# Optimization experiments

Hardware: AMD Instinct MI355X
Metric: run time of the kernel (lower is better)

## Reference

```python
import jax, jax.numpy as jnp
import numpy as np

HIDDEN = 4096
N_HEADS = 32
N_KV = 8
HEAD_DIM = HIDDEN // N_HEADS  # 128
Q_SIZE = N_HEADS * HEAD_DIM   # 4096
KV_SIZE = N_KV * HEAD_DIM     # 1024
ROPE_THETA = 10000.0
B, S = 2, 2048


def _rope_cos_sin(positions):
    # positions: [B,S] int. inv_freq: [HEAD_DIM//2]
    inv_freq = 1.0 / (ROPE_THETA ** (jnp.arange(0, HEAD_DIM, 2, dtype=jnp.float32) / HEAD_DIM))
    ang = positions.astype(jnp.float32)[..., None] * inv_freq  # [B,S,D/2]
    return jnp.cos(ang), jnp.sin(ang)


def _apply_rope_neox(x, cos, sin):
    # x: [B,S,H,D]; neox style: rotate halves
    d2 = HEAD_DIM // 2
    x1, x2 = x[..., :d2], x[..., d2:]
    c = cos[:, :, None, :]
    s = sin[:, :, None, :]
    return jnp.concatenate([x1 * c - x2 * s, x2 * c + x1 * s], axis=-1)


def setup_inputs() -> dict:
    key = jax.random.key(0)
    k1, k2, k3 = jax.random.split(key, 3)
    positions = jnp.broadcast_to(jnp.arange(S, dtype=jnp.int32), (B, S))
    hidden_states = jax.random.normal(k1, (B, S, HIDDEN), dtype=jnp.float32)
    w_qkv = jax.random.normal(k2, (HIDDEN, Q_SIZE + 2 * KV_SIZE), dtype=jnp.float32) * (HIDDEN ** -0.5)
    w_o = jax.random.normal(k3, (Q_SIZE, HIDDEN), dtype=jnp.float32) * (Q_SIZE ** -0.5)
    return {"positions": positions, "hidden_states": hidden_states, "w_qkv": w_qkv, "w_o": w_o}


def reference(positions, hidden_states, w_qkv, w_o):
    qkv = hidden_states @ w_qkv  # [B,S,6144]
    q, k, v = jnp.split(qkv, [Q_SIZE, Q_SIZE + KV_SIZE], axis=-1)
    q = q.reshape(B, S, N_HEADS, HEAD_DIM)
    k = k.reshape(B, S, N_KV, HEAD_DIM)
    v = v.reshape(B, S, N_KV, HEAD_DIM)

    cos, sin = _rope_cos_sin(positions)
    q = _apply_rope_neox(q, cos, sin)
    k = _apply_rope_neox(k, cos, sin)

    # GQA: repeat kv heads to match query heads
    rep = N_HEADS // N_KV
    k = jnp.repeat(k, rep, axis=2)  # [B,S,H,D]
    v = jnp.repeat(v, rep, axis=2)

    scale = HEAD_DIM ** -0.5
    scores = jnp.einsum('bqhd,bkhd->bhqk', q, k) * scale  # [B,H,S,S]
    causal = jnp.tril(jnp.ones((S, S), dtype=bool))
    scores = jnp.where(causal[None, None], scores, jnp.float32(-1e30))
    probs = jax.nn.softmax(scores, axis=-1)
    attn = jnp.einsum('bhqk,bkhd->bqhd', probs, v).reshape(B, S, Q_SIZE)
    return attn @ w_o  # [B,S,HIDDEN]
```

## Files before the change

### kernel.cpp

```cpp
#include <hip/hip_runtime.h>
#include <stdint.h>
#include <stddef.h>


typedef short short8 __attribute__((ext_vector_type(8)));
typedef float f32x4  __attribute__((ext_vector_type(4)));

__device__ __forceinline__ float bf2f(short s) {
    union { uint32_t u; float f; } v;
    v.u = ((uint32_t)(uint16_t)s) << 16;
    return v.f;
}
__device__ __forceinline__ short f2bf(float f) {
    union { float f; uint32_t u; } v;
    v.f = f;
    uint32_t u = v.u;
    uint32_t r = (u + 0x7FFFu + ((u >> 16) & 1u)) >> 16;
    return (short)(uint16_t)r;
}
__device__ __forceinline__ short8 ldcvt8(const float* p) {
    float4 a = *(const float4*)p;
    float4 b = *(const float4*)(p + 4);
    short8 r;
    r[0] = f2bf(a.x); r[1] = f2bf(a.y); r[2] = f2bf(a.z); r[3] = f2bf(a.w);
    r[4] = f2bf(b.x); r[5] = f2bf(b.y); r[6] = f2bf(b.z); r[7] = f2bf(b.w);
    return r;
}
__device__ __forceinline__ void st_out(short* p, float v) { *p = f2bf(v); }
__device__ __forceinline__ void st_out(float* p, float v) { *p = v; }

#define GLDS16(g, l) __builtin_amdgcn_global_load_lds( \
    (const __attribute__((address_space(1))) void*)(g), \
    (__attribute__((address_space(3))) void*)(l), 16, 0, 0)

__global__ __launch_bounds__(256)
void cvt_bf16(const float* __restrict__ in, short* __restrict__ out, int n8)
{
    int i = blockIdx.x * 256 + threadIdx.x;
    int stride = gridDim.x * 256;
    for (; i < n8; i += stride)
        *(short8*)(out + (size_t)i * 8) = ldcvt8(in + (size_t)i * 8);
}

__global__ __launch_bounds__(256)
void transpose_cvt(const float* __restrict__ in, int ldin,
                   short* __restrict__ out, int R, int Cs)
{
    __shared__ short tile[64][72];
    const int bc = blockIdx.x * 64;
    const int br = blockIdx.y * 64;
    const int tid = threadIdx.x;
    const int r  = tid >> 2;
    const int c0 = (tid & 3) * 16;

    const float* src = in + (size_t)(br + r) * ldin + bc + c0;
#pragma unroll
    for (int i = 0; i < 4; i++) {
        float4 v = *(const float4*)(src + 4 * i);
        tile[c0 + 4 * i + 0][r] = f2bf(v.x);
        tile[c0 + 4 * i + 1][r] = f2bf(v.y);
        tile[c0 + 4 * i + 2][r] = f2bf(v.z);
        tile[c0 + 4 * i + 3][r] = f2bf(v.w);
    }
    __syncthreads();

    short* dst = out + (size_t)(bc + r) * R + br + c0;
    *(short8*)(dst)     = *(const short8*)(&tile[r][c0]);
    *(short8*)(dst + 8) = *(const short8*)(&tile[r][c0 + 8]);
}

__global__ __launch_bounds__(256)
void transpose_v(const short* __restrict__ qkv, short* __restrict__ vT)
{
    __shared__ short tile[64][72];
    const int bh = blockIdx.z;
    const int b  = bh >> 3;
    const int hk = bh & 7;
    const int s0 = blockIdx.x * 64;
    const int d0 = blockIdx.y * 64;
    const int tid = threadIdx.x;
    const int r  = tid >> 2;
    const int c0 = (tid & 3) * 16;

    const short* src = qkv + (size_t)(b * 2048 + s0 + r) * 6144 + 5120 + hk * 128 + d0 + c0;
    short8 v0 = *(const short8*)(src);
    short8 v1 = *(const short8*)(src + 8);
#pragma unroll
    for (int i = 0; i < 8; i++) tile[c0 + i][r] = v0[i];
#pragma unroll
    for (int i = 0; i < 8; i++) tile[c0 + 8 + i][r] = v1[i];
    __syncthreads();

    short* dst = vT + ((size_t)bh * 128 + d0 + r) * 2048 + s0 + c0;
    *(short8*)(dst)     = *(const short8*)(&tile[r][c0]);
    *(short8*)(dst + 8) = *(const short8*)(&tile[r][c0 + 8]);
}

__device__ __forceinline__ void stage_tile(const float* __restrict__ Ab, size_t lda,
                                           int kb, short* T, int tid)
{
    const int aRow = tid >> 3;
    const int aChk = tid & 7;
#pragma unroll
    for (int j = 0; j < 4; j++) {
        int row = aRow + 32 * j;
        short8 v = ldcvt8(Ab + (size_t)row * lda + kb + aChk * 8);
        *(short8*)(&T[row * 64 + ((aChk ^ (row & 7)) * 8)]) = v;
    }
}
__device__ __forceinline__ void stage_tile(const short* __restrict__ Ab, size_t lda,
                                           int kb, short* T, int tid)
{
    const int lane = tid & 63;
    const int wave = tid >> 6;
    const int sRow = lane >> 3;
    const int sPhy = lane & 7;
    const int logc = sPhy ^ sRow;
#pragma unroll
    for (int j = 0; j < 4; j++) {
        int row = wave * 32 + j * 8 + sRow;
        const short* g = Ab + (size_t)row * lda + kb + logc * 8;
        GLDS16(g, T + (size_t)(wave * 32 + j * 8) * 64);
    }
}

template <typename AT, typename CT>
__global__ __launch_bounds__(256, 2)
void gemm_tn(const AT* __restrict__ A, int lda, const short* __restrict__ Bt,
             CT* __restrict__ C, int ldc, int M, int N, int K)
{
    __shared__ __align__(16) short As[128 * 64];
    __shared__ __align__(16) short Bs[128 * 64];

    const int tid  = threadIdx.x;
    const int lane = tid & 63;
    const int wave = tid >> 6;
    const int l16  = lane & 15;
    const int quad = lane >> 4;
    const int wm   = wave >> 1;
    const int wn   = wave & 1;

    const int nbx = gridDim.x;
    const int nwg = nbx * gridDim.y;
    int wg = blockIdx.y * nbx + blockIdx.x;
    if ((nwg & 7) == 0) {
        const int cpx = nwg >> 3;
        wg = (wg & 7) * cpx + (wg >> 3);
    }
    const int mb = wg / nbx;
    const int nb = wg - mb * nbx;

    const AT*    Ab = A  + (size_t)mb * 128 * lda;
    const short* Bb = Bt + (size_t)nb * 128 * K;

    f32x4 acc[4][4];
#pragma unroll
    for (int i = 0; i < 4; i++)
#pragma unroll
        for (int j = 0; j < 4; j++) acc[i][j] = {0.f, 0.f, 0.f, 0.f};

    for (int kb = 0; kb < K; kb += 64) {
        __syncthreads();
        stage_tile(Ab, (size_t)lda, kb, As, tid);
        stage_tile(Bb, (size_t)K,   kb, Bs, tid);
        __syncthreads();

#pragma unroll
        for (int ks = 0; ks < 2; ks++) {
            short8 af[4], bf[4];
#pragma unroll
            for (int t = 0; t < 4; t++) {
                int ar = wm * 64 + t * 16 + l16;
                int br = wn * 64 + t * 16 + l16;
                af[t] = *(const short8*)(&As[ar * 64 + (((ks * 4 + quad) ^ (ar & 7)) * 8)]);
                bf[t] = *(const short8*)(&Bs[br * 64 + (((ks * 4 + quad) ^ (br & 7)) * 8)]);
            }
#pragma unroll
            for (int mt = 0; mt < 4; mt++)
#pragma unroll
                for (int nt = 0; nt < 4; nt++)
                    acc[mt][nt] = __builtin_amdgcn_mfma_f32_16x16x32_bf16(
                        af[mt], bf[nt], acc[mt][nt], 0, 0, 0);
        }
    }

#pragma unroll
    for (int mt = 0; mt < 4; mt++)
#pragma unroll
        for (int nt = 0; nt < 4; nt++)
#pragma unroll
            for (int r = 0; r < 4; r++) {
                int row = mb * 128 + wm * 64 + mt * 16 + quad * 4 + r;
                int col = nb * 128 + wn * 64 + nt * 16 + l16;
                st_out(&C[(size_t)row * ldc + col], acc[mt][nt][r]);
            }
}

__global__ __launch_bounds__(256)
void rope_kernel(const int* __restrict__ positions, short* __restrict__ qkv)
{
    const int tok = blockIdx.x;
    const float fp = (float)positions[tok];
    short* base = qkv + (size_t)tok * 6144;
    const float c0 = 0.14391156516f;

    const int d = threadIdx.x & 63;
    const float inv = __expf(-(float)d * c0);
    const float ang = fp * inv;
    float s, c;
    __sincosf(ang, &s, &c);

    for (int head = threadIdx.x >> 6; head < 40; head += 4) {
        int off = (head < 32) ? head * 128 : 4096 + (head - 32) * 128;
        float x1 = bf2f(base[off + d]);
        float x2 = bf2f(base[off + d + 64]);
        base[off + d]      = f2bf(x1 * c - x2 * s);
        base[off + d + 64] = f2bf(x2 * c + x1 * s);
    }
}

__global__ __launch_bounds__(256, 2)
void attn_kernel(short* __restrict__ qkv, const short* __restrict__ vT)
{
    __shared__ __align__(16) short Ks[2][64 * 128];
    __shared__ __align__(16) short Vs[2][128 * 64];
    __shared__ __align__(16) short Pw[4][16][72];

    const int blk = blockIdx.x;
    const int qb  = blk & 31;
    const int h   = (blk >> 5) & 31;
    const int b   = blk >> 10;
    const int hk  = h >> 2;

    const int tid  = threadIdx.x;
    const int lane = tid & 63;
    const int wave = tid >> 6;
    const int l16  = lane & 15;
    const int quad = lane >> 4;

    const size_t ld = 6144;
    const short* Kbase = qkv + (size_t)b * 2048 * ld + 4096 + hk * 128;
    const short* Vtb   = vT + (size_t)(b * 8 + hk) * 128 * 2048;

    short8 qf[4];
    {
        const short* Qp = qkv + (size_t)(b * 2048 + qb * 64 + wave * 16 + l16) * ld + h * 128;
#pragma unroll
        for (int ks = 0; ks < 4; ks++)
            qf[ks] = *(const short8*)(Qp + ks * 32 + quad * 8);
    }

    f32x4 oacc[8];
#pragma unroll
    for (int g = 0; g < 8; g++) oacc[g] = {0.f, 0.f, 0.f, 0.f};
    float mrow[4] = {-1e30f, -1e30f, -1e30f, -1e30f};
    float lrow[4] = {0.f, 0.f, 0.f, 0.f};
    const float scale = 0.08838834764831845f;

    const int sRowK = lane >> 4;
    const int sPhyK = lane & 15;
    const int sRowV = lane >> 3;
    const int sPhyV = lane & 7;

    auto stageK = [&](int buf, int kt) {
#pragma unroll
        for (int i = 0; i < 4; i++) {
            int row  = wave * 16 + i * 4 + sRowK;
            int logc = sPhyK ^ (row & 15);
            GLDS16(Kbase + (size_t)(kt * 64 + row) * ld + logc * 8,
                   &Ks[buf][(wave * 16 + i * 4) * 128]);
        }
    };
    auto stageV = [&](int buf, int kt) {
#pragma unroll
        for (int i = 0; i < 4; i++) {
            int row  = wave * 32 + i * 8 + sRowV;
            int logc = sPhyV ^ (row & 7);
            GLDS16(Vtb + (size_t)row * 2048 + kt * 64 + logc * 8,
                   &Vs[buf][(wave * 32 + i * 8) * 64]);
        }
    };

    stageK(0, 0);
    stageV(0, 0);

    int cur = 0;
    for (int kt = 0; kt <= qb; kt++) {
        __syncthreads();
        if (kt < qb) { stageK(cur ^ 1, kt + 1); stageV(cur ^ 1, kt + 1); }

        f32x4 sacc[4];
        __builtin_amdgcn_s_setprio(1);
#pragma unroll
        for (int g = 0; g < 4; g++) {
            sacc[g] = {0.f, 0.f, 0.f, 0.f};
#pragma unroll
            for (int ks = 0; ks < 4; ks++) {
                int row  = l16 + 16 * g;
                int phys = (ks * 4 + quad) ^ l16;
                short8 kf = *(const short8*)(&Ks[cur][row * 128 + phys * 8]);
                sacc[g] = __builtin_amdgcn_mfma_f32_16x16x32_bf16(qf[ks], kf, sacc[g], 0, 0, 0);
            }
        }
        __builtin_amdgcn_s_setprio(0);

        const int srow_base = qb * 64 + wave * 16 + quad * 4;
        const bool diag = (kt == qb);
        float sv[4][4];
#pragma unroll
        for (int g = 0; g < 4; g++)
#pragma unroll
            for (int r = 0; r < 4; r++) {
                float x = sacc[g][r] * scale;
                if (diag) {
                    int t = kt * 64 + g * 16 + l16;
                    if (t > srow_base + r) x = -1e30f;
                }
                sv[g][r] = x;
            }

        float mx[4];
#pragma unroll
        for (int r = 0; r < 4; r++) {
            float m0 = fmaxf(fmaxf(sv[0][r], sv[1][r]), fmaxf(sv[2][r], sv[3][r]));
#pragma unroll
            for (int off = 1; off < 16; off <<= 1)
                m0 = fmaxf(m0, __shfl_xor(m0, off, 64));
            mx[r] = m0;
        }
        int grow = 0;
#pragma unroll
        for (int r = 0; r < 4; r++) grow |= (mx[r] > mrow[r] + 8.f) ? 1 : 0;
        if (__any(grow)) {
#pragma unroll
            for (int r = 0; r < 4; r++) {
                float mn = fmaxf(mrow[r], mx[r]);
                float al = __expf(mrow[r] - mn);
                mrow[r] = mn;
                lrow[r] *= al;
#pragma unroll
                for (int gd = 0; gd < 8; gd++) oacc[gd][r] *= al;
            }
        }
#pragma unroll
        for (int r = 0; r < 4; r++) {
            float rs = 0.f;
#pragma unroll
            for (int g = 0; g < 4; g++) {
                float p = __expf(sv[g][r] - mrow[r]);
                sv[g][r] = p;
                rs += p;
            }
#pragma unroll
            for (int off = 1; off < 16; off <<= 1)
                rs += __shfl_xor(rs, off, 64);
            lrow[r] += rs;
        }

#pragma unroll
        for (int g = 0; g < 4; g++)
#pragma unroll
            for (int r = 0; r < 4; r++)
                Pw[wave][quad * 4 + r][l16 + 16 * g] = f2bf(sv[g][r]);
        asm volatile("s_waitcnt lgkmcnt(0)" ::: "memory");
        __builtin_amdgcn_sched_barrier(0);

        __builtin_amdgcn_s_setprio(1);
#pragma unroll
        for (int ks = 0; ks < 2; ks++) {
            short8 af = *(const short8*)(&Pw[wave][l16][ks * 32 + quad * 8]);
#pragma unroll
            for (int gd = 0; gd < 8; gd++) {
                int row  = l16 + 16 * gd;
                int phys = (ks * 4 + quad) ^ (l16 & 7);
                short8 vf = *(const short8*)(&Vs[cur][row * 64 + phys * 8]);
                oacc[gd] = __builtin_amdgcn_mfma_f32_16x16x32_bf16(af, vf, oacc[gd], 0, 0, 0);
            }
        }
        __builtin_amdgcn_s_setprio(0);
        cur ^= 1;
    }

    const int srow_base = qb * 64 + wave * 16 + quad * 4;
#pragma unroll
    for (int r = 0; r < 4; r++) {
        float inv = 1.0f / lrow[r];
        size_t rowoff = (size_t)(b * 2048 + srow_base + r) * ld + h * 128;
#pragma unroll
        for (int gd = 0; gd < 8; gd++)
            qkv[rowoff + gd * 16 + l16] = f2bf(oacc[gd][r] * inv);
    }
}

extern "C" void kernel_launch(void* const* d_in, const int* in_sizes, int n_in,
                              void* d_out, int out_size, void* d_ws, size_t ws_size,
                              hipStream_t stream)
{
    const int*   positions = (const int*)d_in[0];
    const float* hidden    = (const float*)d_in[1];
    const float* w_qkv     = (const float*)d_in[2];
    const float* w_o       = (const float*)d_in[3];
    float* out = (float*)d_out;

    short* qkv = (short*)d_ws;
    short* wT  = qkv + (size_t)4096 * 6144;
    short* vT  = wT;
    short* hB  = wT + (size_t)4096 * 4096;

    const size_t need = ((size_t)4096 * 6144 + (size_t)4096 * 4096 * 2) * sizeof(short);
    const bool cvtA = (ws_size >= need);

    if (cvtA) {
        cvt_bf16<<<2048, 256, 0, stream>>>(hidden, hB, 4096 * 4096 / 8);
        for (int c = 0; c < 2; c++) {
            transpose_cvt<<<dim3(48, 64), 256, 0, stream>>>(
                w_qkv + c * 3072, 6144, wT, 4096, 3072);
            gemm_tn<short, short><<<dim3(24, 32), 256, 0, stream>>>(
                hB, 4096, wT, qkv + c * 3072, 6144, 4096, 3072, 4096);
        }
    } else {
        for (int c = 0; c < 2; c++) {
            transpose_cvt<<<dim3(48, 64), 256, 0, stream>>>(
                w_qkv + c * 3072, 6144, wT, 4096, 3072);
            gemm_tn<float, short><<<dim3(24, 32), 256, 0, stream>>>(
                hidden, 4096, wT, qkv + c * 3072, 6144, 4096, 3072, 4096);
        }
    }
    transpose_v<<<dim3(32, 2, 16), 256, 0, stream>>>(qkv, vT);
    rope_kernel<<<4096, 256, 0, stream>>>(positions, qkv);
    attn_kernel<<<2048, 256, 0, stream>>>(qkv, vT);
    transpose_cvt<<<dim3(64, 64), 256, 0, stream>>>(w_o, 4096, wT, 4096, 4096);
    gemm_tn<short, float><<<dim3(32, 32), 256, 0, stream>>>(
        qkv, 6144, wT, out, 4096, 4096, 4096, 4096);
}
```

Baseline: 920.7 us.

## Pair low and high causal query blocks per workgroup and transpose score MFMA

Each workgroup now processes query block p together with block 31-p, which evens out causal work across the 1024 blocks and lets both blocks reuse the same staged K/V tiles. The score MFMA operands are swapped so each lane holds one query row's scores. Row max and sum then need only two cross-lane shuffles instead of four per row, and P is written to LDS as packed 4-element vectors. The cost is doubled accumulator and Q-fragment registers, which may reduce occupancy or cause spills under launch_bounds(256,2), and half as many workgroups are launched.

```diff
diff --git a/kernel.cpp b/kernel.cpp
--- a/kernel.cpp
+++ b/kernel.cpp
@@ -4,6 +4,7 @@
 
 
 typedef short short8 __attribute__((ext_vector_type(8)));
+typedef short short4v __attribute__((ext_vector_type(4)));
 typedef float f32x4  __attribute__((ext_vector_type(4)));
 
 __device__ __forceinline__ float bf2f(short s) {
@@ -219,6 +220,97 @@
     }
 }
 
+__device__ __forceinline__ void attn_tile(
+    const short* __restrict__ Ksb, const short* __restrict__ Vsb,
+    short* __restrict__ PwW, const short8 qf[4], f32x4 oacc[8],
+    float& mrow, float& lrow, int tok0, int qrow, bool diag,
+    int l16, int quad)
+{
+    const float scale = 0.08838834764831845f;
+
+    f32x4 sacc[4];
+    __builtin_amdgcn_s_setprio(1);
+#pragma unroll
+    for (int g = 0; g < 4; g++) {
+        sacc[g] = {0.f, 0.f, 0.f, 0.f};
+#pragma unroll
+        for (int ks = 0; ks < 4; ks++) {
+            int row  = l16 + 16 * g;
+            int phys = (ks * 4 + quad) ^ l16;
+            short8 kf = *(const short8*)(&Ksb[row * 128 + phys * 8]);
+            sacc[g] = __builtin_amdgcn_mfma_f32_16x16x32_bf16(kf, qf[ks], sacc[g], 0, 0, 0);
+        }
+    }
+    __builtin_amdgcn_s_setprio(0);
+
+    float sv[4][4];
+    float mx = -1e30f;
+#pragma unroll
+    for (int g = 0; g < 4; g++)
+#pragma unroll
+        for (int r = 0; r < 4; r++) {
+            float x = sacc[g][r] * scale;
+            if (diag) {
+                int t = tok0 + g * 16 + quad * 4 + r;
+                if (t > qrow) x = -1e30f;
+            }
+            sv[g][r] = x;
+            mx = fmaxf(mx, x);
+        }
+    mx = fmaxf(mx, __shfl_xor(mx, 16, 64));
+    mx = fmaxf(mx, __shfl_xor(mx, 32, 64));
+
+    if (__any(mx > mrow + 8.f)) {
+        float mn = fmaxf(mrow, mx);
+        float al = __expf(mrow - mn);
+        mrow = mn;
+        lrow *= al;
+#pragma unroll
+        for (int r = 0; r < 4; r++) {
+            float alr = __shfl(al, quad * 4 + r, 64);
+#pragma unroll
+            for (int gd = 0; gd < 8; gd++) oacc[gd][r] *= alr;
+        }
+    }
+
+    float rs = 0.f;
+#pragma unroll
+    for (int g = 0; g < 4; g++)
+#pragma unroll
+        for (int r = 0; r < 4; r++) {
+            float p = __expf(sv[g][r] - mrow);
+            sv[g][r] = p;
+            rs += p;
+        }
+    rs += __shfl_xor(rs, 16, 64);
+    rs += __shfl_xor(rs, 32, 64);
+    lrow += rs;
+
+#pragma unroll
+    for (int g = 0; g < 4; g++) {
+        short4v pk;
+        pk[0] = f2bf(sv[g][0]); pk[1] = f2bf(sv[g][1]);
+        pk[2] = f2bf(sv[g][2]); pk[3] = f2bf(sv[g][3]);
+        *(short4v*)(&PwW[l16 * 72 + g * 16 + quad * 4]) = pk;
+    }
+    asm volatile("s_waitcnt lgkmcnt(0)" ::: "memory");
+    __builtin_amdgcn_sched_barrier(0);
+
+    __builtin_amdgcn_s_setprio(1);
+#pragma unroll
+    for (int ks = 0; ks < 2; ks++) {
+        short8 af = *(const short8*)(&PwW[l16 * 72 + ks * 32 + quad * 8]);
+#pragma unroll
+        for (int gd = 0; gd < 8; gd++) {
+            int row  = l16 + 16 * gd;
+            int phys = (ks * 4 + quad) ^ (l16 & 7);
+            short8 vf = *(const short8*)(&Vsb[row * 64 + phys * 8]);
+            oacc[gd] = __builtin_amdgcn_mfma_f32_16x16x32_bf16(af, vf, oacc[gd], 0, 0, 0);
+        }
+    }
+    __builtin_amdgcn_s_setprio(0);
+}
+
 __global__ __launch_bounds__(256, 2)
 void attn_kernel(short* __restrict__ qkv, const short* __restrict__ vT)
 {
@@ -227,10 +319,12 @@
     __shared__ __align__(16) short Pw[4][16][72];
 
     const int blk = blockIdx.x;
-    const int qb  = blk & 31;
-    const int h   = (blk >> 5) & 31;
-    const int b   = blk >> 10;
+    const int p   = blk & 15;
+    const int h   = (blk >> 4) & 31;
+    const int b   = blk >> 9;
     const int hk  = h >> 2;
+    const int qbL = p;
+    const int qbH = 31 - p;
 
     const int tid  = threadIdx.x;
     const int lane = tid & 63;
@@ -241,21 +335,26 @@
     const size_t ld = 6144;
     const short* Kbase = qkv + (size_t)b * 2048 * ld + 4096 + hk * 128;
     const short* Vtb   = vT + (size_t)(b * 8 + hk) * 128 * 2048;
-
-    short8 qf[4];
+    short* PwW = &Pw[wave][0][0];
+
+    short8 qfL[4], qfH[4];
     {
-        const short* Qp = qkv + (size_t)(b * 2048 + qb * 64 + wave * 16 + l16) * ld + h * 128;
-#pragma unroll
-        for (int ks = 0; ks < 4; ks++)
-            qf[ks] = *(const short8*)(Qp + ks * 32 + quad * 8);
-    }
-
-    f32x4 oacc[8];
-#pragma unroll
-    for (int g = 0; g < 8; g++) oacc[g] = {0.f, 0.f, 0.f, 0.f};
-    float mrow[4] = {-1e30f, -1e30f, -1e30f, -1e30f};
-    float lrow[4] = {0.f, 0.f, 0.f, 0.f};
-    const float scale = 0.08838834764831845f;
+        const short* QpL = qkv + (size_t)(b * 2048 + qbL * 64 + wave * 16 + l16) * ld + h * 128;
+        const short* QpH = qkv + (size_t)(b * 2048 + qbH * 64 + wave * 16 + l16) * ld + h * 128;
+#pragma unroll
+        for (int ks = 0; ks < 4; ks++) {
+            qfL[ks] = *(const short8*)(QpL + ks * 32 + quad * 8);
+            qfH[ks] = *(const short8*)(QpH + ks * 32 + quad * 8);
+        }
+    }
+
+    f32x4 oaccL[8], oaccH[8];
+#pragma unroll
+    for (int g = 0; g < 8; g++) { oaccL[g] = {0.f,0.f,0.f,0.f}; oaccH[g] = {0.f,0.f,0.f,0.f}; }
+    float mL = -1e30f, lL = 0.f, mH = -1e30f, lH = 0.f;
+
+    const int qrowL = qbL * 64 + wave * 16 + l16;
+    const int qrowH = qbH * 64 + wave * 16 + l16;
 
     const int sRowK = lane >> 4;
     const int sPhyK = lane & 15;
@@ -285,110 +384,29 @@
     stageV(0, 0);
 
     int cur = 0;
-    for (int kt = 0; kt <= qb; kt++) {
+    for (int kt = 0; kt <= qbH; kt++) {
         __syncthreads();
-        if (kt < qb) { stageK(cur ^ 1, kt + 1); stageV(cur ^ 1, kt + 1); }
-
-        f32x4 sacc[4];
-        __builtin_amdgcn_s_setprio(1);
-#pragma unroll
-        for (int g = 0; g < 4; g++) {
-            sacc[g] = {0.f, 0.f, 0.f, 0.f};
-#pragma unroll
-            for (int ks = 0; ks < 4; ks++) {
-                int row  = l16 + 16 * g;
-                int phys = (ks * 4 + quad) ^ l16;
-                short8 kf = *(const short8*)(&Ks[cur][row * 128 + phys * 8]);
-                sacc[g] = __builtin_amdgcn_mfma_f32_16x16x32_bf16(qf[ks], kf, sacc[g], 0, 0, 0);
-            }
-        }
-        __builtin_amdgcn_s_setprio(0);
-
-        const int srow_base = qb * 64 + wave * 16 + quad * 4;
-        const bool diag = (kt == qb);
-        float sv[4][4];
-#pragma unroll
-        for (int g = 0; g < 4; g++)
-#pragma unroll
-            for (int r = 0; r < 4; r++) {
-                float x = sacc[g][r] * scale;
-                if (diag) {
-                    int t = kt * 64 + g * 16 + l16;
-                    if (t > srow_base + r) x = -1e30f;
-                }
-                sv[g][r] = x;
-            }
-
-        float mx[4];
-#pragma unroll
-        for (int r = 0; r < 4; r++) {
-            float m0 = fmaxf(fmaxf(sv[0][r], sv[1][r]), fmaxf(sv[2][r], sv[3][r]));
-#pragma unroll
-            for (int off = 1; off < 16; off <<= 1)
-                m0 = fmaxf(m0, __shfl_xor(m0, off, 64));
-            mx[r] = m0;
-        }
-        int grow = 0;
-#pragma unroll
-        for (int r = 0; r < 4; r++) grow |= (mx[r] > mrow[r] + 8.f) ? 1 : 0;
-        if (__any(grow)) {
-#pragma unroll
-            for (int r = 0; r < 4; r++) {
-                float mn = fmaxf(mrow[r], mx[r]);
-                float al = __expf(mrow[r] - mn);
-                mrow[r] = mn;
-                lrow[r] *= al;
-#pragma unroll
-                for (int gd = 0; gd < 8; gd++) oacc[gd][r] *= al;
-            }
-        }
-#pragma unroll
-        for (int r = 0; r < 4; r++) {
-            float rs = 0.f;
-#pragma unroll
-            for (int g = 0; g < 4; g++) {
-                float p = __expf(sv[g][r] - mrow[r]);
-                sv[g][r] = p;
-                rs += p;
-            }
-#pragma unroll
-            for (int off = 1; off < 16; off <<= 1)
-                rs += __shfl_xor(rs, off, 64);
-            lrow[r] += rs;
-        }
-
-#pragma unroll
-        for (int g = 0; g < 4; g++)
-#pragma unroll
-            for (int r = 0; r < 4; r++)
-                Pw[wave][quad * 4 + r][l16 + 16 * g] = f2bf(sv[g][r]);
-        asm volatile("s_waitcnt lgkmcnt(0)" ::: "memory");
-        __builtin_amdgcn_sched_barrier(0);
-
-        __builtin_amdgcn_s_setprio(1);
-#pragma unroll
-        for (int ks = 0; ks < 2; ks++) {
-            short8 af = *(const short8*)(&Pw[wave][l16][ks * 32 + quad * 8]);
-#pragma unroll
-            for (int gd = 0; gd < 8; gd++) {
-                int row  = l16 + 16 * gd;
-                int phys = (ks * 4 + quad) ^ (l16 & 7);
-                short8 vf = *(const short8*)(&Vs[cur][row * 64 + phys * 8]);
-                oacc[gd] = __builtin_amdgcn_mfma_f32_16x16x32_bf16(af, vf, oacc[gd], 0, 0, 0);
-            }
-        }
-        __builtin_amdgcn_s_setprio(0);
+        if (kt < qbH) { stageK(cur ^ 1, kt + 1); stageV(cur ^ 1, kt + 1); }
+
+        attn_tile(&Ks[cur][0], &Vs[cur][0], PwW, qfH, oaccH, mH, lH,
+                  kt * 64, qrowH, kt == qbH, l16, quad);
+        if (kt <= qbL)
+            attn_tile(&Ks[cur][0], &Vs[cur][0], PwW, qfL, oaccL, mL, lL,
+                      kt * 64, qrowL, kt == qbL, l16, quad);
         cur ^= 1;
     }
 
-    const int srow_base = qb * 64 + wave * 16 + quad * 4;
 #pragma unroll
     for (int r = 0; r < 4; r++) {
-        float inv = 1.0f / lrow[r];
-        size_t rowoff = (size_t)(b * 2048 + srow_base + r) * ld + h * 128;
-#pragma unroll
-        for (int gd = 0; gd < 8; gd++)
-            qkv[rowoff + gd * 16 + l16] = f2bf(oacc[gd][r] * inv);
+        float liH = 1.0f / __shfl(lH, quad * 4 + r, 64);
+        float liL = 1.0f / __shfl(lL, quad * 4 + r, 64);
+        size_t rowH = (size_t)(b * 2048 + qbH * 64 + wave * 16 + quad * 4 + r) * ld + h * 128;
+        size_t rowL = (size_t)(b * 2048 + qbL * 64 + wave * 16 + quad * 4 + r) * ld + h * 128;
+#pragma unroll
+        for (int gd = 0; gd < 8; gd++) {
+            qkv[rowH + gd * 16 + l16] = f2bf(oaccH[gd][r] * liH);
+            qkv[rowL + gd * 16 + l16] = f2bf(oaccL[gd][r] * liL);
+        }
     }
 }
 
@@ -428,7 +446,7 @@
     }
     transpose_v<<<dim3(32, 2, 16), 256, 0, stream>>>(qkv, vT);
     rope_kernel<<<4096, 256, 0, stream>>>(positions, qkv);
-    attn_kernel<<<2048, 256, 0, stream>>>(qkv, vT);
+    attn_kernel<<<1024, 256, 0, stream>>>(qkv, vT);
     transpose_cvt<<<dim3(64, 64), 256, 0, stream>>>(w_o, 4096, wT, 4096, 4096);
     gemm_tn<short, float><<<dim3(32, 32), 256, 0, stream>>>(
         qkv, 6144, wT, out, 4096, 4096, 4096, 4096);
```

New measurement: 768.1 us. 1.2x faster.
